# Performance work log

Measured on AMD Instinct MI355X. Metric: run time of the kernel, lower is better.

The kernel has to match this reference:

```python
import jax, jax.numpy as jnp
import numpy as np

B, T, C = 4, 2048, 768
NH, NKV, HD = 12, 12, 64
RMS_EPS = 1e-6


def rms_norm(x):
    return x * jax.lax.rsqrt(jnp.mean(x * x, axis=-1, keepdims=True) + RMS_EPS)


def apply_rotary_emb(x, cos, sin):
    # x: [B,T,H,D], cos/sin: [T,D/2]
    d2 = x.shape[-1] // 2
    x1, x2 = x[..., :d2], x[..., d2:]
    c = cos[None, :, None, :]
    s = sin[None, :, None, :]
    return jnp.concatenate([x1 * c - x2 * s, x1 * s + x2 * c], axis=-1)


def setup_inputs() -> dict:
    key = jax.random.key(0)
    ks = jax.random.split(key, 10)
    inv_freq = 1.0 / (100000.0 ** (np.arange(0, HD, 2, dtype=np.float32) / HD))  # [HD/2]
    t = np.arange(T, dtype=np.float32)
    freqs = np.outer(t, inv_freq)  # [T, HD/2]
    return {
        "x": jax.random.normal(ks[0], (B, T, C), jnp.float32),
        "ve": jax.random.normal(ks[1], (B, T, C), jnp.float32),
        "cos": jnp.asarray(np.cos(freqs)),
        "sin": jnp.asarray(np.sin(freqs)),
        "Wq": jax.random.normal(ks[2], (C, C), jnp.float32) * (1.0 / np.sqrt(C)),
        "Wk": jax.random.normal(ks[3], (C, C), jnp.float32) * (1.0 / np.sqrt(C)),
        "Wv": jax.random.normal(ks[4], (C, C), jnp.float32) * (1.0 / np.sqrt(C)),
        "Wproj": jax.random.normal(ks[5], (C, C), jnp.float32) * (1.0 / np.sqrt(C)),
        "Wgate": jax.random.normal(ks[6], (NKV, 12), jnp.float32) * 0.1,
        "window_left": 1024,
    }


def reference(x, ve, cos, sin, Wq, Wk, Wv, Wproj, Wgate, window_left):
    q = (x @ Wq.T).reshape(B, T, NH, HD)
    k = (x @ Wk.T).reshape(B, T, NKV, HD)
    v = (x @ Wv.T).reshape(B, T, NKV, HD)

    # value-embedding gating (has_ve path): gate = 3*sigmoid(Linear(x[...,:12]))
    ve_h = ve.reshape(B, T, NKV, HD)
    gate = 3.0 * jax.nn.sigmoid(x[..., :12] @ Wgate.T)  # [B,T,NKV]
    v = v + gate[..., None] * ve_h

    q = apply_rotary_emb(q, cos, sin)
    k = apply_rotary_emb(k, cos, sin)
    q = rms_norm(q) * 1.2
    k = rms_norm(k) * 1.2

    # sliding-window causal bias
    row = jnp.arange(T)[:, None]
    col = jnp.arange(T)[None, :]
    mask = (row >= col) & ((row - col) <= window_left)
    bias = jnp.where(mask, 0.0, -1e9).astype(x.dtype)  # [T,T]

    scale = 1.0 / np.sqrt(HD)
    att = jnp.einsum("bqhd,bkhd->bhqk", q, k) * scale + bias[None, None]
    att = jax.nn.softmax(att, axis=-1)
    y = jnp.einsum("bhqk,bkhd->bqhd", att, v).reshape(B, T, C)
    return y @ Wproj.T
```

## Files before the change

kernel.cpp:

```cpp
#include <hip/hip_runtime.h>
#include <hip/hip_bf16.h>
#include <cstdint>
#include <cstddef>

#define B_  4
#define T_  2048
#define C_  768
#define NH_ 12
#define HD_ 64

typedef __bf16 bf16_t;
typedef __attribute__((ext_vector_type(8))) __bf16 bf16x8;
typedef __attribute__((ext_vector_type(4))) __bf16 bf16x4;
typedef __attribute__((ext_vector_type(4))) float floatx4;
typedef __attribute__((ext_vector_type(8))) unsigned short ushort8;

#define MFMA16(a, b, c) __builtin_amdgcn_mfma_f32_16x16x32_bf16((a), (b), (c), 0, 0, 0)

#define SM_C1 0.18033688f
#define SM_C2 -17.3123405f

typedef const __attribute__((address_space(1))) uint8_t* gptr_t;
typedef __attribute__((address_space(3))) uint8_t* lptr_t;

static __device__ __forceinline__ void gld16(const void* g, void* l) {
    __builtin_amdgcn_global_load_lds((gptr_t)g, (lptr_t)l, 16, 0, 0);
}

static __device__ __forceinline__ float bfl(unsigned p) {
    return __builtin_bit_cast(float, p << 16);
}
static __device__ __forceinline__ float bfh(unsigned p) {
    return __builtin_bit_cast(float, p & 0xffff0000u);
}

__global__ __launch_bounds__(256) void cvt_all_kernel(
    const void* s0, const void* s1, const void* s2, const void* s3,
    const void* s4, const void* s5, const void* s6, const void* s7, const void* s8,
    bf16_t* d0, bf16_t* d1, bf16_t* d2, bf16_t* d3,
    bf16_t* d4, bf16_t* d5, bf16_t* d6, bf16_t* d7, bf16_t* d8)
{
    const bool isf32 = (((const unsigned short*)s2)[0] == 0);
    if (!isf32) return;
    const void* srcs[9] = {s0, s1, s2, s3, s4, s5, s6, s7, s8};
    bf16_t*     dsts[9] = {d0, d1, d2, d3, d4, d5, d6, d7, d8};
    const int   ns[9]   = {B_*T_*C_, B_*T_*C_, T_*32, T_*32,
                           C_*C_, C_*C_, C_*C_, C_*C_, 144};
    const int t = blockIdx.y;
    const float* sf = (const float*)srcs[t];
    bf16_t*     dst = dsts[t];
    const int   nc  = ns[t] >> 3;
    const int stride = gridDim.x * 256;
    for (int i = blockIdx.x * 256 + threadIdx.x; i < nc; i += stride) {
        ushort8 o;
#pragma unroll
        for (int j = 0; j < 8; j++)
            o[j] = (unsigned short)__builtin_bit_cast(unsigned short,
                     (bf16_t)sf[i * 8 + j]);
        *(ushort8*)&dst[i * 8] = o;
    }
}

__global__ __launch_bounds__(256, 3) void gemm_qkv_fused(
    const void* xr,  const bf16_t* xc,
    const void* wqr, const bf16_t* wqc,
    const void* wkr, const bf16_t* wkc,
    const void* wvr, const bf16_t* wvc,
    const void* cr,  const bf16_t* ccv,
    const void* sr,  const bf16_t* scv,
    const void* ver, const bf16_t* vec,
    const void* wgr, const bf16_t* wgc,
    bf16_t* qn, bf16_t* kn, bf16_t* vt)
{
    __shared__ alignas(16) char sm[36864];
    const bool f32 = (((const unsigned short*)cr)[0] == 0);
    const bf16_t* X  = f32 ? xc  : (const bf16_t*)xr;
    const bf16_t* WQ = f32 ? wqc : (const bf16_t*)wqr;
    const bf16_t* WK = f32 ? wkc : (const bf16_t*)wkr;
    const bf16_t* WV = f32 ? wvc : (const bf16_t*)wvr;
    const bf16_t* CC = f32 ? ccv : (const bf16_t*)cr;
    const bf16_t* SS = f32 ? scv : (const bf16_t*)sr;
    const bf16_t* VE = f32 ? vec : (const bf16_t*)ver;
    const bf16_t* WG = f32 ? wgc : (const bf16_t*)wgr;

    const int sel = blockIdx.y / 6;
    const int nt  = blockIdx.y % 6;
    const int m0  = blockIdx.x * 128;
    const int n0  = nt * 128;
    const bf16_t* Bm = (sel == 0) ? WQ : (sel == 1) ? WK : WV;

    bf16_t* As = (bf16_t*)sm;
    bf16_t* Bs = (bf16_t*)(sm + 16384);

    const int tid  = threadIdx.x;
    const int lane = tid & 63;
    const int wid  = tid >> 6;
    const int m16  = lane & 15;
    const int quad = lane >> 4;
    const int wm   = (wid >> 1) * 64;
    const int wn   = (wid & 1) * 64;
    const int srow = lane >> 2;
    const int soct = (lane & 3) * 8;

    floatx4 acc[4][4];
#pragma unroll
    for (int i = 0; i < 4; i++)
#pragma unroll
        for (int j = 0; j < 4; j++) acc[i][j] = (floatx4){0.f, 0.f, 0.f, 0.f};

    for (int k0 = 0; k0 < C_; k0 += 64) {
        const bf16_t* ga0 = &X[(size_t)(m0 + 16 * wid + srow) * C_ + k0 + soct];
        const bf16_t* gb0 = &Bm[(size_t)(n0 + 16 * wid + srow) * C_ + k0 + soct];
        gld16(ga0,                        As + wid * 512);
        gld16(ga0 + (size_t)64 * C_,      As + wid * 512 + 2048);
        gld16(gb0,                        Bs + wid * 512);
        gld16(gb0 + (size_t)64 * C_,      Bs + wid * 512 + 2048);
        gld16(ga0 + 32,                   As + 4096 + wid * 512);
        gld16(ga0 + (size_t)64 * C_ + 32, As + 4096 + wid * 512 + 2048);
        gld16(gb0 + 32,                   Bs + 4096 + wid * 512);
        gld16(gb0 + (size_t)64 * C_ + 32, Bs + 4096 + wid * 512 + 2048);
        __syncthreads();
#pragma unroll
        for (int half = 0; half < 2; half++) {
            bf16x8 af[4], bfr[4];
#pragma unroll
            for (int i = 0; i < 4; i++)
                af[i] = *(const bf16x8*)&As[half * 4096 + (wm + i * 16 + m16) * 32 + quad * 8];
#pragma unroll
            for (int j = 0; j < 4; j++)
                bfr[j] = *(const bf16x8*)&Bs[half * 4096 + (wn + j * 16 + m16) * 32 + quad * 8];
#pragma unroll
            for (int i = 0; i < 4; i++)
#pragma unroll
                for (int j = 0; j < 4; j++)
                    acc[i][j] = MFMA16(af[i], bfr[j], acc[i][j]);
        }
        __syncthreads();
    }

    if (sel < 2) {
        unsigned* csT = (unsigned*)sm;
        const int tbase = m0 & 2047;
        for (int idx = tid; idx < 128 * 32; idx += 256) {
            const int rr = idx >> 5, dd = idx & 31;
            const unsigned cv = ((const unsigned short*)CC)[(tbase + rr) * 32 + dd];
            const unsigned sv = ((const unsigned short*)SS)[(tbase + rr) * 32 + dd];
            csT[rr * 33 + dd] = cv | (sv << 16);
        }
        __syncthreads();
        bf16_t* OUT = (sel == 0) ? qn : kn;
#pragma unroll
        for (int i = 0; i < 4; i++) {
            float c0[4], s0[4], c1[4], s1[4];
#pragma unroll
            for (int r = 0; r < 4; r++) {
                const int rl = wm + i * 16 + quad * 4 + r;
                const unsigned p0 = csT[rl * 33 + m16];
                const unsigned p1 = csT[rl * 33 + 16 + m16];
                c0[r] = bfl(p0); s0[r] = bfh(p0);
                c1[r] = bfl(p1); s1[r] = bfh(p1);
            }
            floatx4 r0, r1, r2, r3;
            float ss[4];
#pragma unroll
            for (int r = 0; r < 4; r++) {
                r0[r] = acc[i][0][r] * c0[r] - acc[i][2][r] * s0[r];
                r1[r] = acc[i][1][r] * c1[r] - acc[i][3][r] * s1[r];
                r2[r] = acc[i][0][r] * s0[r] + acc[i][2][r] * c0[r];
                r3[r] = acc[i][1][r] * s1[r] + acc[i][3][r] * c1[r];
                ss[r] = r0[r]*r0[r] + r1[r]*r1[r] + r2[r]*r2[r] + r3[r]*r3[r];
            }
#pragma unroll
            for (int r = 0; r < 4; r++) {
#pragma unroll
                for (int off = 1; off < 16; off <<= 1)
                    ss[r] += __shfl_xor(ss[r], off, 64);
            }
#pragma unroll
            for (int r = 0; r < 4; r++) {
                const float scl = rsqrtf(ss[r] * (1.f / 64.f) + 1e-6f) * 1.2f;
                const size_t rowoff = (size_t)(m0 + wm + i * 16 + quad * 4 + r) * C_
                                      + n0 + wn + m16;
                OUT[rowoff]      = (bf16_t)(r0[r] * scl);
                OUT[rowoff + 16] = (bf16_t)(r1[r] * scl);
                OUT[rowoff + 32] = (bf16_t)(r2[r] * scl);
                OUT[rowoff + 48] = (bf16_t)(r3[r] * scl);
            }
        }
    } else {
        bf16_t* veT = (bf16_t*)sm;
        float*  gT  = (float*)(sm + 34816);
        for (int idx = tid; idx < 2048; idx += 256) {
            const int rr = idx >> 4, ch = idx & 15;
            *(bf16x8*)&veT[rr * 136 + ch * 8] =
                *(const bf16x8*)&VE[(size_t)(m0 + rr) * C_ + n0 + ch * 8];
        }
        {
            const int row = tid & 127, hh = tid >> 7;
            const int head = nt * 2 + hh;
            float g = 0.f;
#pragma unroll
            for (int j2 = 0; j2 < 12; j2++)
                g += (float)X[(size_t)(m0 + row) * C_ + j2] * (float)WG[head * 12 + j2];
            gT[hh * 128 + row] = 3.f / (1.f + __expf(-g));
        }
        __syncthreads();
        const int hh2  = wn >> 6;
        const int head = nt * 2 + hh2;
        const int bb = m0 >> 11, t0 = m0 & 2047;
#pragma unroll
        for (int i = 0; i < 4; i++) {
            const floatx4 gr = *(const floatx4*)&gT[hh2 * 128 + wm + i * 16 + quad * 4];
            const int tslot = t0 + wm + (i >> 1) * 32 + quad * 8 + (i & 1) * 4;
#pragma unroll
            for (int j = 0; j < 4; j++) {
                bf16x4 o;
#pragma unroll
                for (int r = 0; r < 4; r++) {
                    const float vef = (float)veT[(wm + i * 16 + quad * 4 + r) * 136
                                                 + wn + j * 16 + m16];
                    o[r] = (bf16_t)(acc[i][j][r] + gr[r] * vef);
                }
                *(bf16x4*)&vt[((size_t)(bb * NH_ + head) * HD_ + j * 16 + m16) * T_
                              + tslot] = o;
            }
        }
    }
}

template <bool OUT_BF16>
__device__ __forceinline__ void gemm_bt_tile(
    const bf16_t* __restrict__ A, const bf16_t* __restrict__ Bm,
    void* __restrict__ Cout, int m0, int n0, int K, int ldc)
{
    __shared__ bf16_t As[2][128 * 32];
    __shared__ bf16_t Bs[2][128 * 32];
    const int tid  = threadIdx.x;
    const int lane = tid & 63;
    const int wid  = tid >> 6;
    const int m16  = lane & 15;
    const int quad = lane >> 4;
    const int wm   = (wid >> 1) * 64;
    const int wn   = (wid & 1) * 64;
    const int srow = lane >> 2;
    const int soct = (lane & 3) * 8;

    floatx4 acc[4][4];
#pragma unroll
    for (int i = 0; i < 4; i++)
#pragma unroll
        for (int j = 0; j < 4; j++) acc[i][j] = (floatx4){0.f, 0.f, 0.f, 0.f};

    for (int k0 = 0; k0 < K; k0 += 64) {
        const bf16_t* ga0 = &A[(size_t)(m0 + 16 * wid + srow) * K + k0 + soct];
        const bf16_t* gb0 = &Bm[(size_t)(n0 + 16 * wid + srow) * K + k0 + soct];
        gld16(ga0,                       (bf16_t*)As[0] + wid * 512);
        gld16(ga0 + (size_t)64 * K,      (bf16_t*)As[0] + wid * 512 + 2048);
        gld16(gb0,                       (bf16_t*)Bs[0] + wid * 512);
        gld16(gb0 + (size_t)64 * K,      (bf16_t*)Bs[0] + wid * 512 + 2048);
        gld16(ga0 + 32,                  (bf16_t*)As[1] + wid * 512);
        gld16(ga0 + (size_t)64 * K + 32, (bf16_t*)As[1] + wid * 512 + 2048);
        gld16(gb0 + 32,                  (bf16_t*)Bs[1] + wid * 512);
        gld16(gb0 + (size_t)64 * K + 32, (bf16_t*)Bs[1] + wid * 512 + 2048);
        __syncthreads();
#pragma unroll
        for (int half = 0; half < 2; half++) {
            bf16x8 af[4], bfr[4];
#pragma unroll
            for (int i = 0; i < 4; i++)
                af[i] = *(const bf16x8*)&As[half][(wm + i * 16 + m16) * 32 + quad * 8];
#pragma unroll
            for (int j = 0; j < 4; j++)
                bfr[j] = *(const bf16x8*)&Bs[half][(wn + j * 16 + m16) * 32 + quad * 8];
#pragma unroll
            for (int i = 0; i < 4; i++)
#pragma unroll
                for (int j = 0; j < 4; j++)
                    acc[i][j] = MFMA16(af[i], bfr[j], acc[i][j]);
        }
        __syncthreads();
    }
#pragma unroll
    for (int i = 0; i < 4; i++) {
#pragma unroll
        for (int j = 0; j < 4; j++) {
            const int colg = n0 + wn + j * 16 + m16;
#pragma unroll
            for (int r = 0; r < 4; r++) {
                const int rowg = m0 + wm + i * 16 + quad * 4 + r;
                if (OUT_BF16)
                    ((bf16_t*)Cout)[(size_t)rowg * ldc + colg] = (bf16_t)acc[i][j][r];
                else
                    ((float*)Cout)[(size_t)rowg * ldc + colg] = acc[i][j][r];
            }
        }
    }
}

__global__ __launch_bounds__(256, 3) void gemm_proj_kernel(
    const bf16_t* __restrict__ yb, const void* wpr, const bf16_t* wpc,
    void* __restrict__ out, const void* cr)
{
    const bool f32 = (((const unsigned short*)cr)[0] == 0);
    const bf16_t* WP = f32 ? wpc : (const bf16_t*)wpr;
    if (f32)
        gemm_bt_tile<false>(yb, WP, out, blockIdx.x * 128, blockIdx.y * 128, C_, C_);
    else
        gemm_bt_tile<true>(yb, WP, out, blockIdx.x * 128, blockIdx.y * 128, C_, C_);
}

__global__ __launch_bounds__(256, 3) void attn_kernel(
    const bf16_t* __restrict__ Q, const bf16_t* __restrict__ Km,
    const bf16_t* __restrict__ Vtg, bf16_t* __restrict__ Y,
    const int* __restrict__ wl)
{
    const int o   = blockIdx.x;
    const int xcd = o & 7;
    const int idx = o >> 3;
    const int lb  = idx >> 4;
    const int qs  = idx & 15;
    const int bh  = xcd * 6 + lb;
    const int v   = lb % 3;
    int qblk;
    if (v == 0)      qblk = qs;
    else if (v == 1) qblk = 15 - qs;
    else             qblk = (int)((0xECA8642013579BDFull >> (qs * 4)) & 0xF);
    const int q0 = qblk * 128;
    const int b  = bh / NH_;
    const int h  = bh % NH_;
    const int window = wl[0];
    const int tid  = threadIdx.x;
    const int wid  = tid >> 6;
    const int lane = tid & 63;
    const int m16  = lane & 15;
    const int quad = lane >> 4;
    const int qw   = q0 + wid * 32;

    const bf16_t* Qb = Q + (size_t)b * T_ * C_ + h * HD_;
    const bf16_t* Kb = Km + (size_t)b * T_ * C_ + h * HD_;
    const bf16_t* Vb = Vtg + (size_t)bh * HD_ * T_;

    __shared__ bf16_t Ks[2][64 * 64];
    __shared__ bf16_t Vs[2][64 * 64];

    bf16x8 qf[2][2];
#pragma unroll
    for (int mt = 0; mt < 2; mt++)
#pragma unroll
        for (int ks = 0; ks < 2; ks++)
            qf[mt][ks] = *(const bf16x8*)
                &Qb[(size_t)(qw + mt * 16 + m16) * C_ + ks * 32 + quad * 8];

    const int srow = tid >> 2;
    const int soct = tid & 3;
    const int g0   = 2 * soct, g1 = 2 * soct + 1;
    const int kd0  = srow * 64 + ((g0 ^ (srow & 7)) << 3);
    const int kd1  = srow * 64 + ((g1 ^ (srow & 7)) << 3);
    int rsw[2];
#pragma unroll
    for (int ks = 0; ks < 2; ks++)
        rsw[ks] = (((ks * 4 + quad) ^ (m16 & 7)) << 3);

    int lo = q0 - window;
    if (lo < 0) lo = 0;
    lo &= ~63;
    const int nch = (q0 + 128 - lo) >> 6;

    floatx4 accO[2][4];
#pragma unroll
    for (int mt = 0; mt < 2; mt++)
#pragma unroll
        for (int dt = 0; dt < 4; dt++) accO[mt][dt] = (floatx4){0.f, 0.f, 0.f, 0.f};
    floatx4 accS[2];
    accS[0] = (floatx4){0.f, 0.f, 0.f, 0.f};
    accS[1] = (floatx4){0.f, 0.f, 0.f, 0.f};
    const bf16x4 zero4 = {(bf16_t)0.f, (bf16_t)0.f, (bf16_t)0.f, (bf16_t)0.f};
    const bf16x8 ones8 = {(bf16_t)1.f, (bf16_t)1.f, (bf16_t)1.f, (bf16_t)1.f,
                          (bf16_t)1.f, (bf16_t)1.f, (bf16_t)1.f, (bf16_t)1.f};

    bf16x8 ka0 = *(const bf16x8*)&Kb[(size_t)(lo + srow) * C_ + g0 * 8];
    bf16x8 ka1 = *(const bf16x8*)&Kb[(size_t)(lo + srow) * C_ + g1 * 8];
    bf16x8 va0 = *(const bf16x8*)&Vb[(size_t)srow * T_ + lo + g0 * 8];
    bf16x8 va1 = *(const bf16x8*)&Vb[(size_t)srow * T_ + lo + g1 * 8];
    *(bf16x8*)&Ks[0][kd0] = ka0;
    *(bf16x8*)&Ks[0][kd1] = ka1;
    *(bf16x8*)&Vs[0][kd0] = va0;
    *(bf16x8*)&Vs[0][kd1] = va1;

    for (int ic = 0; ic < nch; ic++) {
        const int kc = lo + ic * 64;
        const bool more = (ic + 1 < nch);
        if (more) {
            const int kn2 = kc + 64;
            ka0 = *(const bf16x8*)&Kb[(size_t)(kn2 + srow) * C_ + g0 * 8];
            ka1 = *(const bf16x8*)&Kb[(size_t)(kn2 + srow) * C_ + g1 * 8];
            va0 = *(const bf16x8*)&Vb[(size_t)srow * T_ + kn2 + g0 * 8];
            va1 = *(const bf16x8*)&Vb[(size_t)srow * T_ + kn2 + g1 * 8];
        }
        __syncthreads();
        const int buf = ic & 1;

        const bool skip = (kc > qw + 31) || (kc + 63 < qw - window);
        if (!skip) {
            bf16x8 kf[4][2];
#pragma unroll
            for (int nt = 0; nt < 4; nt++) {
                const int rb = (nt * 16 + m16) * 64;
                kf[nt][0] = *(const bf16x8*)&Ks[buf][rb + rsw[0]];
                kf[nt][1] = *(const bf16x8*)&Ks[buf][rb + rsw[1]];
            }
            bf16x4 pk[2][4];
            unsigned livemask = 0;
#pragma unroll
            for (int mt = 0; mt < 2; mt++) {
                const int qmin = qw + mt * 16, qmax = qmin + 15;
#pragma unroll
                for (int nt = 0; nt < 4; nt++) {
                    const int kmin = kc + nt * 16, kmax = kmin + 15;
                    if (kmin > qmax || kmax < qmin - window) {
                        pk[mt][nt] = zero4;
                        continue;
                    }
                    livemask |= 1u << (mt * 4 + nt);
                    floatx4 z = (floatx4){0.f, 0.f, 0.f, 0.f};
                    z = MFMA16(kf[nt][0], qf[mt][0], z);
                    z = MFMA16(kf[nt][1], qf[mt][1], z);
                    const bool edge = (kmax > qmin) || (kmin < qmax - window);
                    const int query = qmin + m16;
                    bf16x4 t4;
#pragma unroll
                    for (int r = 0; r < 4; r++) {
                        float p = __builtin_amdgcn_exp2f(
                            fmaf(z[r], SM_C1, SM_C2));
                        if (edge) {
                            const int key = kmin + quad * 4 + r;
                            const bool ok = (key <= query) &&
                                            (query - key <= window);
                            p = ok ? p : 0.f;
                        }
                        t4[r] = (bf16_t)p;
                    }
                    pk[mt][nt] = t4;
                }
            }
#pragma unroll
            for (int pr = 0; pr < 2; pr++) {
                const unsigned pm0 = (livemask >> (2 * pr)) & 3u;
                const unsigned pm1 = (livemask >> (4 + 2 * pr)) & 3u;
                if (!(pm0 | pm1)) continue;
                const bf16x8 pa0 = __builtin_shufflevector(
                    pk[0][2 * pr], pk[0][2 * pr + 1], 0, 1, 2, 3, 4, 5, 6, 7);
                const bf16x8 pa1 = __builtin_shufflevector(
                    pk[1][2 * pr], pk[1][2 * pr + 1], 0, 1, 2, 3, 4, 5, 6, 7);
                const int vco = (((pr * 4 + quad) ^ (m16 & 7)) << 3);
                if (pm0) accS[0] = MFMA16(pa0, ones8, accS[0]);
                if (pm1) accS[1] = MFMA16(pa1, ones8, accS[1]);
#pragma unroll
                for (int dt = 0; dt < 4; dt++) {
                    const bf16x8 vf = *(const bf16x8*)
                        &Vs[buf][(dt * 16 + m16) * 64 + vco];
                    if (pm0) accO[0][dt] = MFMA16(pa0, vf, accO[0][dt]);
                    if (pm1) accO[1][dt] = MFMA16(pa1, vf, accO[1][dt]);
                }
            }
        }

        if (more) {
            const int nb = buf ^ 1;
            *(bf16x8*)&Ks[nb][kd0] = ka0;
            *(bf16x8*)&Ks[nb][kd1] = ka1;
            *(bf16x8*)&Vs[nb][kd0] = va0;
            *(bf16x8*)&Vs[nb][kd1] = va1;
        }
    }

#pragma unroll
    for (int mt = 0; mt < 2; mt++) {
#pragma unroll
        for (int r = 0; r < 4; r++) {
            const float inv = 1.f / accS[mt][r];
            const int   tq  = qw + mt * 16 + quad * 4 + r;
#pragma unroll
            for (int dt = 0; dt < 4; dt++)
                Y[((size_t)b * T_ + tq) * C_ + h * HD_ + dt * 16 + m16] =
                    (bf16_t)(accO[mt][dt][r] * inv);
        }
    }
}

extern "C" void kernel_launch(void* const* d_in, const int* in_sizes, int n_in,
                              void* d_out, int out_size, void* d_ws, size_t ws_size,
                              hipStream_t stream)
{
    const void* x_raw   = d_in[0];
    const void* ve_raw  = d_in[1];
    const void* cos_raw = d_in[2];
    const void* sin_raw = d_in[3];
    const void* wq_raw  = d_in[4];
    const void* wk_raw  = d_in[5];
    const void* wv_raw  = d_in[6];
    const void* wp_raw  = d_in[7];
    const void* wg_raw  = d_in[8];
    const int*  wl      = (const int*)d_in[9];

    const size_t NTC = (size_t)B_ * T_ * C_;
    const size_t WSZ = (size_t)C_ * C_;

    bf16_t* ws  = (bf16_t*)d_ws;
    bf16_t* xb  = ws;
    bf16_t* veb = xb + NTC;
    bf16_t* cb  = veb + NTC;
    bf16_t* sb  = cb + T_ * 32;
    bf16_t* wqb = sb + T_ * 32;
    bf16_t* wkb = wqb + WSZ;
    bf16_t* wvb = wkb + WSZ;
    bf16_t* wpb = wvb + WSZ;
    bf16_t* wgb = wpb + WSZ;
    bf16_t* qn  = wgb + 256;
    bf16_t* kn  = qn + NTC;
    bf16_t* vt  = kn + NTC;
    bf16_t* yb  = vt + NTC;

    cvt_all_kernel<<<dim3(128, 9), 256, 0, stream>>>(
        x_raw, ve_raw, cos_raw, sin_raw, wq_raw, wk_raw, wv_raw, wp_raw, wg_raw,
        xb, veb, cb, sb, wqb, wkb, wvb, wpb, wgb);

    gemm_qkv_fused<<<dim3(64, 18), 256, 0, stream>>>(
        x_raw, xb, wq_raw, wqb, wk_raw, wkb, wv_raw, wvb,
        cos_raw, cb, sin_raw, sb, ve_raw, veb, wg_raw, wgb,
        qn, kn, vt);

    attn_kernel<<<dim3(768), 256, 0, stream>>>(qn, kn, vt, yb, wl);

    gemm_proj_kernel<<<dim3(64, 6), 256, 0, stream>>>(yb, wp_raw, wpb, d_out, cos_raw);
}
```

Measured before the change: 235.8 us.

## Software-pipeline attention loop: overlap QK/exp of next chunk with PV of previous

Restructures the sliding-window attention main loop into a two-stage software pipeline. The QK^T and exp for chunk i now run in the same step as the P·V accumulation for chunk i-1, unrolled by two with ping-pong probability registers. V shared memory is triple-buffered so the V tile for the lagging stage stays valid. The goal is to interleave the exp/mask ALU work with MFMA work and hide the latency between the two. The cost is more registers (two sets of P fragments) and more LDS.

```diff
diff --git a/kernel.cpp b/kernel.cpp
--- a/kernel.cpp
+++ b/kernel.cpp
@@ -341,7 +341,7 @@
     const bf16_t* Vb = Vtg + (size_t)bh * HD_ * T_;
 
     __shared__ bf16_t Ks[2][64 * 64];
-    __shared__ bf16_t Vs[2][64 * 64];
+    __shared__ bf16_t Vs[3][64 * 64];
 
     bf16x8 qf[2][2];
 #pragma unroll
@@ -378,101 +378,127 @@
     const bf16x8 ones8 = {(bf16_t)1.f, (bf16_t)1.f, (bf16_t)1.f, (bf16_t)1.f,
                           (bf16_t)1.f, (bf16_t)1.f, (bf16_t)1.f, (bf16_t)1.f};
 
-    bf16x8 ka0 = *(const bf16x8*)&Kb[(size_t)(lo + srow) * C_ + g0 * 8];
-    bf16x8 ka1 = *(const bf16x8*)&Kb[(size_t)(lo + srow) * C_ + g1 * 8];
-    bf16x8 va0 = *(const bf16x8*)&Vb[(size_t)srow * T_ + lo + g0 * 8];
-    bf16x8 va1 = *(const bf16x8*)&Vb[(size_t)srow * T_ + lo + g1 * 8];
-    *(bf16x8*)&Ks[0][kd0] = ka0;
-    *(bf16x8*)&Ks[0][kd1] = ka1;
-    *(bf16x8*)&Vs[0][kd0] = va0;
-    *(bf16x8*)&Vs[0][kd1] = va1;
-
-    for (int ic = 0; ic < nch; ic++) {
-        const int kc = lo + ic * 64;
-        const bool more = (ic + 1 < nch);
-        if (more) {
-            const int kn2 = kc + 64;
-            ka0 = *(const bf16x8*)&Kb[(size_t)(kn2 + srow) * C_ + g0 * 8];
-            ka1 = *(const bf16x8*)&Kb[(size_t)(kn2 + srow) * C_ + g1 * 8];
-            va0 = *(const bf16x8*)&Vb[(size_t)srow * T_ + kn2 + g0 * 8];
-            va1 = *(const bf16x8*)&Vb[(size_t)srow * T_ + kn2 + g1 * 8];
-        }
-        __syncthreads();
-        const int buf = ic & 1;
-
-        const bool skip = (kc > qw + 31) || (kc + 63 < qw - window);
-        if (!skip) {
-            bf16x8 kf[4][2];
-#pragma unroll
-            for (int nt = 0; nt < 4; nt++) {
-                const int rb = (nt * 16 + m16) * 64;
-                kf[nt][0] = *(const bf16x8*)&Ks[buf][rb + rsw[0]];
-                kf[nt][1] = *(const bf16x8*)&Ks[buf][rb + rsw[1]];
-            }
-            bf16x4 pk[2][4];
-            unsigned livemask = 0;
-#pragma unroll
-            for (int mt = 0; mt < 2; mt++) {
-                const int qmin = qw + mt * 16, qmax = qmin + 15;
-#pragma unroll
-                for (int nt = 0; nt < 4; nt++) {
-                    const int kmin = kc + nt * 16, kmax = kmin + 15;
-                    if (kmin > qmax || kmax < qmin - window) {
-                        pk[mt][nt] = zero4;
-                        continue;
-                    }
-                    livemask |= 1u << (mt * 4 + nt);
-                    floatx4 z = (floatx4){0.f, 0.f, 0.f, 0.f};
-                    z = MFMA16(kf[nt][0], qf[mt][0], z);
-                    z = MFMA16(kf[nt][1], qf[mt][1], z);
-                    const bool edge = (kmax > qmin) || (kmin < qmax - window);
-                    const int query = qmin + m16;
-                    bf16x4 t4;
-#pragma unroll
-                    for (int r = 0; r < 4; r++) {
-                        float p = __builtin_amdgcn_exp2f(
-                            fmaf(z[r], SM_C1, SM_C2));
-                        if (edge) {
-                            const int key = kmin + quad * 4 + r;
-                            const bool ok = (key <= query) &&
-                                            (query - key <= window);
-                            p = ok ? p : 0.f;
-                        }
-                        t4[r] = (bf16_t)p;
-                    }
-                    pk[mt][nt] = t4;
-                }
-            }
-#pragma unroll
-            for (int pr = 0; pr < 2; pr++) {
-                const unsigned pm0 = (livemask >> (2 * pr)) & 3u;
-                const unsigned pm1 = (livemask >> (4 + 2 * pr)) & 3u;
-                if (!(pm0 | pm1)) continue;
-                const bf16x8 pa0 = __builtin_shufflevector(
-                    pk[0][2 * pr], pk[0][2 * pr + 1], 0, 1, 2, 3, 4, 5, 6, 7);
-                const bf16x8 pa1 = __builtin_shufflevector(
-                    pk[1][2 * pr], pk[1][2 * pr + 1], 0, 1, 2, 3, 4, 5, 6, 7);
-                const int vco = (((pr * 4 + quad) ^ (m16 & 7)) << 3);
-                if (pm0) accS[0] = MFMA16(pa0, ones8, accS[0]);
-                if (pm1) accS[1] = MFMA16(pa1, ones8, accS[1]);
-#pragma unroll
-                for (int dt = 0; dt < 4; dt++) {
-                    const bf16x8 vf = *(const bf16x8*)
-                        &Vs[buf][(dt * 16 + m16) * 64 + vco];
-                    if (pm0) accO[0][dt] = MFMA16(pa0, vf, accO[0][dt]);
-                    if (pm1) accO[1][dt] = MFMA16(pa1, vf, accO[1][dt]);
-                }
-            }
-        }
-
-        if (more) {
-            const int nb = buf ^ 1;
-            *(bf16x8*)&Ks[nb][kd0] = ka0;
-            *(bf16x8*)&Ks[nb][kd1] = ka1;
-            *(bf16x8*)&Vs[nb][kd0] = va0;
-            *(bf16x8*)&Vs[nb][kd1] = va1;
-        }
-    }
+    bf16x8 ka0, ka1, va0, va1;
+    bf16x4 pkA[2][4], pkB[2][4];
+    unsigned lmA = 0, lmB = 0;
+
+#define STAGEREG(kc2) do {                                                    \
+        ka0 = *(const bf16x8*)&Kb[(size_t)((kc2) + srow) * C_ + g0 * 8];      \
+        ka1 = *(const bf16x8*)&Kb[(size_t)((kc2) + srow) * C_ + g1 * 8];      \
+        va0 = *(const bf16x8*)&Vb[(size_t)srow * T_ + (kc2) + g0 * 8];        \
+        va1 = *(const bf16x8*)&Vb[(size_t)srow * T_ + (kc2) + g1 * 8];        \
+    } while (0)
+
+#define STAGEWRITE(bK, bV) do {                                               \
+        *(bf16x8*)&Ks[bK][kd0] = ka0;                                         \
+        *(bf16x8*)&Ks[bK][kd1] = ka1;                                         \
+        *(bf16x8*)&Vs[bV][kd0] = va0;                                         \
+        *(bf16x8*)&Vs[bV][kd1] = va1;                                         \
+    } while (0)
+
+#define QKEXP(kc, bufK, pk, lm) do {                                          \
+        lm = 0;                                                               \
+        if (!(((kc) > qw + 31) || ((kc) + 63 < qw - window))) {               \
+            bf16x8 kf[4][2];                                                  \
+            _Pragma("unroll")                                                 \
+            for (int nt = 0; nt < 4; nt++) {                                  \
+                const int rb = (nt * 16 + m16) * 64;                          \
+                kf[nt][0] = *(const bf16x8*)&Ks[bufK][rb + rsw[0]];           \
+                kf[nt][1] = *(const bf16x8*)&Ks[bufK][rb + rsw[1]];           \
+            }                                                                 \
+            _Pragma("unroll")                                                 \
+            for (int mt = 0; mt < 2; mt++) {                                  \
+                const int qmin = qw + mt * 16, qmax = qmin + 15;              \
+                _Pragma("unroll")                                             \
+                for (int nt = 0; nt < 4; nt++) {                              \
+                    const int kmin = (kc) + nt * 16, kmax = kmin + 15;        \
+                    if (kmin > qmax || kmax < qmin - window) {                \
+                        pk[mt][nt] = zero4;                                   \
+                        continue;                                             \
+                    }                                                         \
+                    lm |= 1u << (mt * 4 + nt);                                \
+                    floatx4 z = (floatx4){0.f, 0.f, 0.f, 0.f};                \
+                    z = MFMA16(kf[nt][0], qf[mt][0], z);                      \
+                    z = MFMA16(kf[nt][1], qf[mt][1], z);                      \
+                    const bool edge = (kmax > qmin) || (kmin < qmax - window);\
+                    const int query = qmin + m16;                             \
+                    bf16x4 t4;                                                \
+                    _Pragma("unroll")                                         \
+                    for (int r = 0; r < 4; r++) {                             \
+                        float p = __builtin_amdgcn_exp2f(                     \
+                            fmaf(z[r], SM_C1, SM_C2));                        \
+                        if (edge) {                                           \
+                            const int key = kmin + quad * 4 + r;              \
+                            const bool ok = (key <= query) &&                 \
+                                            (query - key <= window);          \
+                            p = ok ? p : 0.f;                                 \
+                        }                                                     \
+                        t4[r] = (bf16_t)p;                                    \
+                    }                                                         \
+                    pk[mt][nt] = t4;                                          \
+                }                                                             \
+            }                                                                 \
+        }                                                                     \
+    } while (0)
+
+#define PVSTEP(lm, pk, bufV) do {                                             \
+        _Pragma("unroll")                                                     \
+        for (int pr = 0; pr < 2; pr++) {                                      \
+            const unsigned pm0 = ((lm) >> (2 * pr)) & 3u;                     \
+            const unsigned pm1 = ((lm) >> (4 + 2 * pr)) & 3u;                 \
+            if (!(pm0 | pm1)) continue;                                       \
+            const bf16x8 pa0 = __builtin_shufflevector(                       \
+                pk[0][2 * pr], pk[0][2 * pr + 1], 0, 1, 2, 3, 4, 5, 6, 7);    \
+            const bf16x8 pa1 = __builtin_shufflevector(                       \
+                pk[1][2 * pr], pk[1][2 * pr + 1], 0, 1, 2, 3, 4, 5, 6, 7);    \
+            const int vco = (((pr * 4 + quad) ^ (m16 & 7)) << 3);             \
+            if (pm0) accS[0] = MFMA16(pa0, ones8, accS[0]);                   \
+            if (pm1) accS[1] = MFMA16(pa1, ones8, accS[1]);                   \
+            _Pragma("unroll")                                                 \
+            for (int dt = 0; dt < 4; dt++) {                                  \
+                const bf16x8 vf = *(const bf16x8*)                            \
+                    &Vs[bufV][(dt * 16 + m16) * 64 + vco];                    \
+                if (pm0) accO[0][dt] = MFMA16(pa0, vf, accO[0][dt]);          \
+                if (pm1) accO[1][dt] = MFMA16(pa1, vf, accO[1][dt]);          \
+            }                                                                 \
+        }                                                                     \
+    } while (0)
+
+    STAGEREG(lo);
+    STAGEWRITE(0, 0);
+    STAGEREG(lo + 64);
+    __syncthreads();
+    QKEXP(lo, 0, pkA, lmA);
+    STAGEWRITE(1, 1);
+
+    int i = 1;
+    for (; i + 1 < nch; i += 2) {
+        __syncthreads();
+        const int kci = lo + i * 64;
+        STAGEREG(kci + 64);
+        QKEXP(kci, (i & 1), pkB, lmB);
+        PVSTEP(lmA, pkA, (i + 2) % 3);
+        STAGEWRITE((i + 1) & 1, (i + 1) % 3);
+
+        __syncthreads();
+        const int kcj = kci + 64;
+        STAGEREG(kcj + 64);
+        QKEXP(kcj, ((i + 1) & 1), pkA, lmA);
+        PVSTEP(lmB, pkB, i % 3);
+        STAGEWRITE((i + 2) & 1, (i + 2) % 3);
+    }
+    {
+        __syncthreads();
+        const int kci = lo + i * 64;
+        QKEXP(kci, (i & 1), pkB, lmB);
+        PVSTEP(lmA, pkA, (i + 2) % 3);
+    }
+    PVSTEP(lmB, pkB, i % 3);
+
+#undef STAGEREG
+#undef STAGEWRITE
+#undef QKEXP
+#undef PVSTEP
 
 #pragma unroll
     for (int mt = 0; mt < 2; mt++) {
```

Result: slower. 280.4 us (+18.9%).
